# Kernel optimization log

Measured on AMD Instinct MI355X. Metric: run time of the kernel, lower is better.

## Reference

```python
import jax, jax.numpy as jnp
import numpy as np

E = 8          # n_experts
TOP_K = 2      # n_active_experts


def setup_inputs() -> dict:
    key = jax.random.key(0)
    ks = jax.random.split(key, 9)
    B, S, D, H = 4, 2048, 2048, 1408
    w = 0.02  # weight scale for numerical stability
    return {
        "x": jax.random.normal(ks[0], (B, S, D), dtype=jnp.float32),
        "gate_w": jax.random.normal(ks[1], (E, D), dtype=jnp.float32) * w,
        "expert_bias": jnp.zeros((E,), dtype=jnp.float32),
        "Wg": jax.random.normal(ks[2], (E, H, D), dtype=jnp.float32) * w,
        "Wu": jax.random.normal(ks[3], (E, H, D), dtype=jnp.float32) * w,
        "Wd": jax.random.normal(ks[4], (E, D, H), dtype=jnp.float32) * w,
        "Ws_g": jax.random.normal(ks[5], (H, D), dtype=jnp.float32) * w,
        "Ws_u": jax.random.normal(ks[6], (H, D), dtype=jnp.float32) * w,
        "Ws_d": jax.random.normal(ks[7], (D, H), dtype=jnp.float32) * w,
    }


def _swiglu(x, wg, wu, wd):
    # torch Linear layout: y = x @ W.T
    return (jax.nn.silu(x @ wg.T) * (x @ wu.T)) @ wd.T


def reference(x, gate_w, expert_bias, Wg, Wu, Wd, Ws_g, Ws_u, Ws_d):
    B, S, D = x.shape
    flat = x.reshape(-1, D)                      # [N, D]
    N = flat.shape[0]

    logits = flat @ gate_w.T                     # [N, E]
    probs = jax.nn.softmax(logits, axis=-1)
    biased = logits + expert_bias
    _, top_idx = jax.lax.top_k(biased, TOP_K)    # [N, K] (bias used only for selection)
    top_w = jnp.take_along_axis(probs, top_idx, axis=-1)
    top_w = top_w / jnp.sum(top_w, axis=-1, keepdims=True)

    # dense per-token combine weights: cw[n, e] = sum_k top_w[n,k] * (top_idx[n,k]==e)
    rows = jnp.arange(N)[:, None]
    cw = jnp.zeros((N, E), dtype=flat.dtype).at[rows, top_idx].add(top_w)

    out = jnp.zeros_like(flat)
    for e in range(E):  # fixed small expert count; equivalent to gather/scatter dispatch
        out = out + cw[:, e:e + 1] * _swiglu(flat, Wg[e], Wu[e], Wd[e])

    out = out + _swiglu(flat, Ws_g, Ws_u, Ws_d)  # shared expert
    return out.reshape(B, S, D)
```

## Files before the change

### kernel.cpp

```cpp
#include <hip/hip_runtime.h>
#include <hip/hip_bf16.h>

#define N_TOK 8192
#define DDIM  2048
#define HDIM  1408
#define ROWS_R 16384
#define ROWS_T 24576
#define MAXTILES 104
#define BM 256
#define BK 64

typedef unsigned short u16;
typedef unsigned int   u32;
typedef __bf16 bf16x8 __attribute__((ext_vector_type(8)));
typedef float  f32x4  __attribute__((ext_vector_type(4)));

__device__ __forceinline__ u16 f2bf(float f) {
  union { float f; u32 u; } v; v.f = f;
  u32 u = v.u;
  return (u16)((u + 0x7fffu + ((u >> 16) & 1u)) >> 16);
}
__device__ __forceinline__ float bf2f(u16 b) {
  union { u32 u; float f; } v; v.u = ((u32)b) << 16; return v.f;
}

typedef __attribute__((address_space(1))) void gvoid;
typedef __attribute__((address_space(3))) void lvoid;
__device__ __forceinline__ void gload16(const void* g, void* l) {
  __builtin_amdgcn_global_load_lds((gvoid*)g, (lvoid*)l, 16, 0, 0);
}

#define BAR __builtin_amdgcn_s_barrier()
#define SP1 __builtin_amdgcn_s_setprio(1)
#define SP0 __builtin_amdgcn_s_setprio(0)
#define LGK0 do { asm volatile("s_waitcnt lgkmcnt(0)" ::: "memory"); \
                  __builtin_amdgcn_sched_barrier(0); } while (0)
#define VMCNT(n) asm volatile("s_waitcnt vmcnt(" #n ")" ::: "memory")

#define READ_A8(base, mb) { \
  _Pragma("unroll") for (int m_ = 0; m_ < 4; ++m_) { \
    int r_ = wr * 128 + ((mb) + m_) * 16 + l15; \
    _Pragma("unroll") for (int kk_ = 0; kk_ < 2; ++kk_) { \
      int cch_ = kk_ * 4 + lhi; \
      af[m_ * 2 + kk_] = *(const bf16x8*)((const char*)(base) + r_ * 128 + ((cch_ ^ (r_ & 7)) * 16)); } } }

#define READ_B4(base, nb) { \
  _Pragma("unroll") for (int n_ = 0; n_ < 2; ++n_) { \
    int r_ = wc * 64 + ((nb) + n_) * 16 + l15; \
    _Pragma("unroll") for (int kk_ = 0; kk_ < 2; ++kk_) { \
      int cch_ = kk_ * 4 + lhi; \
      bf[((nb) + n_) * 2 + kk_] = *(const bf16x8*)((const char*)(base) + r_ * 128 + ((cch_ ^ (r_ & 7)) * 16)); } } }

#define MM16(mb, nb) { \
  _Pragma("unroll") for (int m_ = 0; m_ < 4; ++m_) \
  _Pragma("unroll") for (int n_ = 0; n_ < 2; ++n_) \
  _Pragma("unroll") for (int kk_ = 0; kk_ < 2; ++kk_) \
    acc[(mb) + m_][(nb) + n_] = __builtin_amdgcn_mfma_f32_16x16x32_bf16( \
        af[m_ * 2 + kk_], bf[((nb) + n_) * 2 + kk_], acc[(mb) + m_][(nb) + n_], 0, 0, 0); }

__global__ void k_gate(const float* __restrict__ x, const float* __restrict__ gw,
                       const float* __restrict__ bias, int* __restrict__ tok_idx,
                       float* __restrict__ wts, int* __restrict__ counts,
                       u16* __restrict__ xb) {
  int lane = threadIdx.x & 63;
  int n = blockIdx.x * 4 + (threadIdx.x >> 6);
  const float* xr = x + (size_t)n * DDIM;
  u16* xbr = xb + (size_t)n * DDIM;
  float acc[8];
#pragma unroll
  for (int e = 0; e < 8; ++e) acc[e] = 0.f;
#pragma unroll 2
  for (int j0 = 0; j0 < DDIM; j0 += 256) {
    float4 xv = *(const float4*)(xr + j0 + lane * 4);
    u32 p0 = (u32)f2bf(xv.x) | ((u32)f2bf(xv.y) << 16);
    u32 p1 = (u32)f2bf(xv.z) | ((u32)f2bf(xv.w) << 16);
    *(uint2*)(xbr + j0 + lane * 4) = make_uint2(p0, p1);
#pragma unroll
    for (int e = 0; e < 8; ++e) {
      float4 gv = *(const float4*)(gw + e * DDIM + j0 + lane * 4);
      acc[e] += xv.x * gv.x + xv.y * gv.y + xv.z * gv.z + xv.w * gv.w;
    }
  }
#pragma unroll
  for (int e = 0; e < 8; ++e) {
#pragma unroll
    for (int off = 32; off > 0; off >>= 1) acc[e] += __shfl_xor(acc[e], off);
  }
  if (lane == 0) {
    float m = acc[0];
    for (int e = 1; e < 8; ++e) m = fmaxf(m, acc[e]);
    float p[8];
    for (int e = 0; e < 8; ++e) p[e] = expf(acc[e] - m);
    float b0[8];
    for (int e = 0; e < 8; ++e) b0[e] = acc[e] + bias[e];
    int i0 = 0;
    for (int e = 1; e < 8; ++e) if (b0[e] > b0[i0]) i0 = e;
    int i1 = (i0 == 0) ? 1 : 0;
    for (int e = 0; e < 8; ++e) if (e != i0 && b0[e] > b0[i1]) i1 = e;
    float w0 = p[i0], w1 = p[i1], inv = 1.f / (w0 + w1);
    tok_idx[2 * n] = i0; tok_idx[2 * n + 1] = i1;
    wts[2 * n] = w0 * inv; wts[2 * n + 1] = w1 * inv;
    atomicAdd(&counts[i0], 1); atomicAdd(&counts[i1], 1);
  }
}

__global__ void k_scan(const int* __restrict__ counts, int* __restrict__ offsets,
                       int* __restrict__ cursors, int* __restrict__ ntiles,
                       int4* __restrict__ tiles) {
  if (threadIdx.x != 0 || blockIdx.x != 0) return;
  int off = 0, idx = 0;
  for (int e = 0; e < 8; ++e) {
    offsets[e] = off; cursors[e] = 0;
    int T = counts[e];
    for (int r = 0; r < T; r += BM) {
      int nr = T - r; if (nr > BM) nr = BM;
      tiles[idx++] = make_int4(e, off + r, nr, 0);
    }
    off += T;
  }
  offsets[8] = off;
  for (int r = 0; r < N_TOK; r += BM)
    tiles[idx++] = make_int4(8, ROWS_R + r, BM, 0);
  *ntiles = idx;
}

__global__ void k_build(const int* __restrict__ tok_idx, const int* __restrict__ offsets,
                        int* __restrict__ cursors, int* __restrict__ token_ids,
                        int* __restrict__ pos) {
  int n = blockIdx.x * blockDim.x + threadIdx.x;
  if (n >= N_TOK) return;
#pragma unroll
  for (int s = 0; s < 2; ++s) {
    int e = tok_idx[2 * n + s];
    int p = offsets[e] + atomicAdd(&cursors[e], 1);
    token_ids[p] = n;
    pos[2 * n + s] = p;
  }
  token_ids[ROWS_R + n] = n;
}

__global__ void k_convall(const float* __restrict__ Wg, const float* __restrict__ Wsg,
                          const float* __restrict__ Wu, const float* __restrict__ Wsu,
                          const float* __restrict__ Wd, const float* __restrict__ Wsd,
                          u16* __restrict__ wgb, u16* __restrict__ wub, u16* __restrict__ wdb) {
  const long PER = (long)9 * HDIM * DDIM / 8;
  const long BIG = (long)8 * HDIM * DDIM / 8;
  const long TOT = 3 * PER;
  long stride = (long)gridDim.x * blockDim.x;
  for (long i = (long)blockIdx.x * blockDim.x + threadIdx.x; i < TOT; i += stride) {
    int g = (int)(i / PER);
    long r = i - (long)g * PER;
    const float* src; u16* dst;
    if (g == 0)      { dst = wgb; src = (r < BIG) ? Wg + r * 8 : Wsg + (r - BIG) * 8; }
    else if (g == 1) { dst = wub; src = (r < BIG) ? Wu + r * 8 : Wsu + (r - BIG) * 8; }
    else             { dst = wdb; src = (r < BIG) ? Wd + r * 8 : Wsd + (r - BIG) * 8; }
    float4 a = ((const float4*)src)[0], b = ((const float4*)src)[1];
    u32 p0 = (u32)f2bf(a.x) | ((u32)f2bf(a.y) << 16);
    u32 p1 = (u32)f2bf(a.z) | ((u32)f2bf(a.w) << 16);
    u32 p2 = (u32)f2bf(b.x) | ((u32)f2bf(b.y) << 16);
    u32 p3 = (u32)f2bf(b.z) | ((u32)f2bf(b.w) << 16);
    ((uint4*)dst)[r] = make_uint4(p0, p1, p2, p3);
  }
}

__global__ __launch_bounds__(512, 2) void k_gemm1(
    const u16* __restrict__ xb, const u16* __restrict__ wgb, const u16* __restrict__ wub,
    const int* __restrict__ token_ids, const int* __restrict__ ntiles,
    const int4* __restrict__ tiles, u16* __restrict__ h) {
  __shared__ u16 As[2][BM * BK];
  __shared__ u16 Bs[2][BM * BK];

  int ntl = *ntiles;
  int nwg = (HDIM / 128) * ntl;
  int bid = blockIdx.x;
  if (bid >= nwg) return;
  int q8 = nwg >> 3, r8 = nwg & 7;
  int xcd = bid & 7, pp = bid >> 3;
  int lid = (xcd < r8 ? xcd * (q8 + 1) : r8 * (q8 + 1) + (xcd - r8) * q8) + pp;
  int bx = lid / ntl, tile = lid - bx * ntl;

  int4 tl = tiles[tile];
  int set = tl.x, grow = tl.y, nrows = tl.z;

  int t = threadIdx.x;
  int wid = t >> 6, lane = t & 63;
  int wr = wid >> 2, wc = wid & 3;
  int l15 = lane & 15, lhi = lane >> 4;

  const u16* aptr[4];
#pragma unroll
  for (int i = 0; i < 4; ++i) {
    int chunk = i * 512 + t;
    int r = chunk >> 3, cc = chunk & 7;
    int c = cc ^ (r & 7);
    int rr = r < nrows ? r : nrows - 1;
    int tok = token_ids[grow + rr];
    aptr[i] = xb + (size_t)tok * DDIM + c * 8;
  }
  const u16* bptr[4];
#pragma unroll
  for (int i = 0; i < 4; ++i) {
    int chunk = i * 512 + t;
    int r = chunk >> 3, cc = chunk & 7;
    int c = cc ^ (r & 7);
    int group = r >> 4;
    int wrow = bx * 128 + (group >> 1) * 16 + (r & 15);
    const u16* base = (group & 1) ? wub : wgb;
    bptr[i] = base + (size_t)set * (HDIM * DDIM) + (size_t)wrow * DDIM + c * 8;
  }

#define ISSUE_A0(b, k0) { gload16(aptr[0] + (k0), (char*)As[b] + (size_t)t * 16); \
                          gload16(aptr[1] + (k0), (char*)As[b] + (size_t)(512 + t) * 16); }
#define ISSUE_A1(b, k0) { gload16(aptr[2] + (k0), (char*)As[b] + (size_t)(1024 + t) * 16); \
                          gload16(aptr[3] + (k0), (char*)As[b] + (size_t)(1536 + t) * 16); }
#define ISSUE_B0(b, k0) { gload16(bptr[0] + (k0), (char*)Bs[b] + (size_t)t * 16); \
                          gload16(bptr[1] + (k0), (char*)Bs[b] + (size_t)(512 + t) * 16); }
#define ISSUE_B1(b, k0) { gload16(bptr[2] + (k0), (char*)Bs[b] + (size_t)(1024 + t) * 16); \
                          gload16(bptr[3] + (k0), (char*)Bs[b] + (size_t)(1536 + t) * 16); }

  f32x4 acc[8][4];
  f32x4 z = {0.f, 0.f, 0.f, 0.f};
#pragma unroll
  for (int m = 0; m < 8; ++m)
#pragma unroll
    for (int n = 0; n < 4; ++n) acc[m][n] = z;

  bf16x8 af[8], bf[8];
  const int NK = DDIM / BK;

  VMCNT(0);
  ISSUE_A0(0, 0); ISSUE_A1(0, 0); ISSUE_B0(0, 0); ISSUE_B1(0, 0);
  VMCNT(0); BAR;

  for (int kt = 0; kt < NK - 1; ++kt) {
    int cur = kt & 1, nxt = cur ^ 1;
    int k1 = (kt + 1) * BK;
    READ_A8(As[cur], 0); READ_B4(Bs[cur], 0);
    ISSUE_A0(nxt, k1); ISSUE_B0(nxt, k1);
    BAR; LGK0;
    SP1; MM16(0, 0); SP0; BAR;
    READ_B4(Bs[cur], 2);
    ISSUE_A1(nxt, k1); ISSUE_B1(nxt, k1);
    BAR; LGK0;
    SP1; MM16(0, 2); SP0; BAR;
    READ_A8(As[cur], 4);
    BAR; LGK0;
    SP1; MM16(4, 0); MM16(4, 2); SP0;
    VMCNT(0); BAR;
  }
  {
    int cur = (NK - 1) & 1;
    READ_A8(As[cur], 0); READ_B4(Bs[cur], 0); READ_B4(Bs[cur], 2);
    LGK0;
    SP1; MM16(0, 0); MM16(0, 2); SP0;
    READ_A8(As[cur], 4);
    LGK0;
    SP1; MM16(4, 0); MM16(4, 2); SP0;
  }

#pragma unroll
  for (int m = 0; m < 8; ++m) {
#pragma unroll
    for (int j = 0; j < 2; ++j) {
      int col = bx * 128 + (wc * 2 + j) * 16 + l15;
#pragma unroll
      for (int qq = 0; qq < 4; ++qq) {
        int rl = wr * 128 + m * 16 + lhi * 4 + qq;
        if (rl < nrows) {
          float g = acc[m][2 * j][qq], u = acc[m][2 * j + 1][qq];
          float hv = g / (1.f + expf(-g)) * u;
          h[(size_t)(grow + rl) * HDIM + col] = f2bf(hv);
        }
      }
    }
  }
#undef ISSUE_A0
#undef ISSUE_A1
#undef ISSUE_B0
#undef ISSUE_B1
}

__global__ __launch_bounds__(512, 2) void k_gemm2(
    const u16* __restrict__ h, const u16* __restrict__ wdb,
    const int* __restrict__ ntiles, const int4* __restrict__ tiles,
    u16* __restrict__ y) {
  __shared__ u16 As[2][BM * BK];
  __shared__ u16 Bs[2][BM * BK];

  int ntl = *ntiles;
  int nwg = (DDIM / 256) * ntl;
  int bid = blockIdx.x;
  if (bid >= nwg) return;
  int q8 = nwg >> 3, r8 = nwg & 7;
  int xcd = bid & 7, pp = bid >> 3;
  int lid = (xcd < r8 ? xcd * (q8 + 1) : r8 * (q8 + 1) + (xcd - r8) * q8) + pp;
  int bx = lid / ntl, tile = lid - bx * ntl;

  int4 tl = tiles[tile];
  int set = tl.x, grow = tl.y, nrows = tl.z;

  int t = threadIdx.x;
  int wid = t >> 6, lane = t & 63;
  int wr = wid >> 2, wc = wid & 3;
  int l15 = lane & 15, lhi = lane >> 4;

  const u16* aptr[4];
  const u16* bptr[4];
#pragma unroll
  for (int i = 0; i < 4; ++i) {
    int chunk = i * 512 + t;
    int r = chunk >> 3, cc = chunk & 7;
    int c = cc ^ (r & 7);
    aptr[i] = h + (size_t)(grow + r) * HDIM + c * 8;
    bptr[i] = wdb + (size_t)set * (DDIM * HDIM) + (size_t)(bx * 256 + r) * HDIM + c * 8;
  }

#define ISSUE_A0(b, k0) { gload16(aptr[0] + (k0), (char*)As[b] + (size_t)t * 16); \
                          gload16(aptr[1] + (k0), (char*)As[b] + (size_t)(512 + t) * 16); }
#define ISSUE_A1(b, k0) { gload16(aptr[2] + (k0), (char*)As[b] + (size_t)(1024 + t) * 16); \
                          gload16(aptr[3] + (k0), (char*)As[b] + (size_t)(1536 + t) * 16); }
#define ISSUE_B0(b, k0) { gload16(bptr[0] + (k0), (char*)Bs[b] + (size_t)t * 16); \
                          gload16(bptr[1] + (k0), (char*)Bs[b] + (size_t)(512 + t) * 16); }
#define ISSUE_B1(b, k0) { gload16(bptr[2] + (k0), (char*)Bs[b] + (size_t)(1024 + t) * 16); \
                          gload16(bptr[3] + (k0), (char*)Bs[b] + (size_t)(1536 + t) * 16); }

  f32x4 acc[8][4];
  f32x4 z = {0.f, 0.f, 0.f, 0.f};
#pragma unroll
  for (int m = 0; m < 8; ++m)
#pragma unroll
    for (int n = 0; n < 4; ++n) acc[m][n] = z;

  bf16x8 af[8], bf[8];
  const int NK2 = HDIM / BK;

  VMCNT(0);
  ISSUE_A0(0, 0); ISSUE_A1(0, 0); ISSUE_B0(0, 0); ISSUE_B1(0, 0);
  VMCNT(0); BAR;

  for (int kt = 0; kt < NK2 - 1; ++kt) {
    int cur = kt & 1, nxt = cur ^ 1;
    int k1 = (kt + 1) * BK;
    READ_A8(As[cur], 0); READ_B4(Bs[cur], 0);
    ISSUE_A0(nxt, k1); ISSUE_B0(nxt, k1);
    BAR; LGK0;
    SP1; MM16(0, 0); SP0; BAR;
    READ_B4(Bs[cur], 2);
    ISSUE_A1(nxt, k1); ISSUE_B1(nxt, k1);
    BAR; LGK0;
    SP1; MM16(0, 2); SP0; BAR;
    READ_A8(As[cur], 4);
    BAR; LGK0;
    SP1; MM16(4, 0); MM16(4, 2); SP0;
    VMCNT(0); BAR;
  }
  {
    int cur = (NK2 - 1) & 1;
    READ_A8(As[cur], 0); READ_B4(Bs[cur], 0); READ_B4(Bs[cur], 2);
    LGK0;
    SP1; MM16(0, 0); MM16(0, 2); SP0;
    READ_A8(As[cur], 4);
    LGK0;
    SP1; MM16(4, 0); MM16(4, 2); SP0;
  }

#pragma unroll
  for (int m = 0; m < 8; ++m) {
#pragma unroll
    for (int n = 0; n < 4; ++n) {
      int col = bx * 256 + wc * 64 + n * 16 + l15;
#pragma unroll
      for (int qq = 0; qq < 4; ++qq) {
        int rl = wr * 128 + m * 16 + lhi * 4 + qq;
        if (rl < nrows)
          y[(size_t)(grow + rl) * DDIM + col] = f2bf(acc[m][n][qq]);
      }
    }
  }
#undef ISSUE_A0
#undef ISSUE_A1
#undef ISSUE_B0
#undef ISSUE_B1
}

__global__ void k_comb(const u16* __restrict__ y, const int* __restrict__ pos,
                       const float* __restrict__ wts, float* __restrict__ out) {
  int n = blockIdx.x;
  int c8 = threadIdx.x;
  int p0 = pos[2 * n], p1 = pos[2 * n + 1];
  float w0 = wts[2 * n], w1 = wts[2 * n + 1];
  uint4 a = ((const uint4*)(y + (size_t)p0 * DDIM))[c8];
  uint4 b = ((const uint4*)(y + (size_t)p1 * DDIM))[c8];
  uint4 c = ((const uint4*)(y + (size_t)(ROWS_R + n) * DDIM))[c8];
  float* o = out + (size_t)n * DDIM + c8 * 8;
#pragma unroll
  for (int j = 0; j < 4; ++j) {
    u32 ua = ((const u32*)&a)[j], ub = ((const u32*)&b)[j], uc = ((const u32*)&c)[j];
    o[2 * j]     = w0 * bf2f((u16)(ua & 0xffff)) + w1 * bf2f((u16)(ub & 0xffff)) + bf2f((u16)(uc & 0xffff));
    o[2 * j + 1] = w0 * bf2f((u16)(ua >> 16))    + w1 * bf2f((u16)(ub >> 16))    + bf2f((u16)(uc >> 16));
  }
}

extern "C" void kernel_launch(void* const* d_in, const int* in_sizes, int n_in,
                              void* d_out, int out_size, void* d_ws, size_t ws_size,
                              hipStream_t stream) {
  const float* x    = (const float*)d_in[0];
  const float* gw   = (const float*)d_in[1];
  const float* bias = (const float*)d_in[2];
  const float* Wg   = (const float*)d_in[3];
  const float* Wu   = (const float*)d_in[4];
  const float* Wd   = (const float*)d_in[5];
  const float* Wsg  = (const float*)d_in[6];
  const float* Wsu  = (const float*)d_in[7];
  const float* Wsd  = (const float*)d_in[8];
  float* out = (float*)d_out;

  char* ws = (char*)d_ws;
  size_t off = 0;
  auto alloc = [&](size_t bytes) -> void* {
    void* p = ws + off;
    off += (bytes + 255) & ~(size_t)255;
    return p;
  };
  u16* xb  = (u16*)alloc((size_t)N_TOK * DDIM * 2);
  u16* wgb = (u16*)alloc((size_t)9 * HDIM * DDIM * 2);
  u16* wub = (u16*)alloc((size_t)9 * HDIM * DDIM * 2);
  u16* wdb = (u16*)alloc((size_t)9 * DDIM * HDIM * 2);
  u16* h   = (u16*)alloc((size_t)ROWS_T * HDIM * 2);
  u16* y   = (u16*)alloc((size_t)ROWS_T * DDIM * 2);
  int*   token_ids = (int*)alloc(ROWS_T * 4);
  int*   tok_idx   = (int*)alloc(N_TOK * 2 * 4);
  int*   pos       = (int*)alloc(N_TOK * 2 * 4);
  float* wts       = (float*)alloc(N_TOK * 2 * 4);
  int*   counts  = (int*)alloc(8 * 4);
  int*   offsets = (int*)alloc(9 * 4);
  int*   cursors = (int*)alloc(8 * 4);
  int*   ntiles  = (int*)alloc(4);
  int4*  tiles   = (int4*)alloc(MAXTILES * 16);

  hipMemsetAsync(counts, 0, 8 * 4, stream);
  k_gate<<<N_TOK / 4, 256, 0, stream>>>(x, gw, bias, tok_idx, wts, counts, xb);
  k_scan<<<1, 64, 0, stream>>>(counts, offsets, cursors, ntiles, tiles);
  k_build<<<(N_TOK + 255) / 256, 256, 0, stream>>>(tok_idx, offsets, cursors, token_ids, pos);

  k_convall<<<4096, 256, 0, stream>>>(Wg, Wsg, Wu, Wsu, Wd, Wsd, wgb, wub, wdb);

  k_gemm1<<<(HDIM / 128) * MAXTILES, 512, 0, stream>>>(xb, wgb, wub, token_ids, ntiles, tiles, h);
  k_gemm2<<<(DDIM / 256) * MAXTILES, 512, 0, stream>>>(h, wdb, ntiles, tiles, y);
  k_comb<<<N_TOK, 256, 0, stream>>>(y, pos, wts, out);
}
```

Measured before the change: 948.0 us.

## Software-pipeline LDS fragment reads across K tiles with double-buffered registers in both GEMMs

Replaces the per-K-tile schedule (read fragments, wait lgkmcnt(0), compute) with a register double-buffered pipeline. A fragments alternate between two register sets by quarter, and B fragments plus the first A quarter of the next tile are prefetched from LDS while the current tile's last MFMAs run. The global-to-LDS loads for the whole next tile are issued in one STAGE call, and barriers drop from five to two per tile. Explicit lgkmcnt waits are gone, so LDS-read ordering is left to the compiler. This adds register pressure under the 512-thread, 2-blocks-per-CU bounds and risks correctness if the odd/even tile unrolling is wrong.

```diff
diff --git a/kernel.cpp b/kernel.cpp
--- a/kernel.cpp
+++ b/kernel.cpp
@@ -30,33 +30,41 @@
   __builtin_amdgcn_global_load_lds((gvoid*)g, (lvoid*)l, 16, 0, 0);
 }
 
-#define BAR __builtin_amdgcn_s_barrier()
+#define BARF asm volatile("s_barrier" ::: "memory")
 #define SP1 __builtin_amdgcn_s_setprio(1)
 #define SP0 __builtin_amdgcn_s_setprio(0)
-#define LGK0 do { asm volatile("s_waitcnt lgkmcnt(0)" ::: "memory"); \
-                  __builtin_amdgcn_sched_barrier(0); } while (0)
+#define SB0 __builtin_amdgcn_sched_barrier(0)
 #define VMCNT(n) asm volatile("s_waitcnt vmcnt(" #n ")" ::: "memory")
 
-#define READ_A8(base, mb) { \
-  _Pragma("unroll") for (int m_ = 0; m_ < 4; ++m_) { \
-    int r_ = wr * 128 + ((mb) + m_) * 16 + l15; \
+#define RDA4(cc, q, dst) { \
+  _Pragma("unroll") for (int m_ = 0; m_ < 2; ++m_) { \
+    int r_ = wr * 128 + ((q) * 2 + m_) * 16 + l15; \
     _Pragma("unroll") for (int kk_ = 0; kk_ < 2; ++kk_) { \
       int cch_ = kk_ * 4 + lhi; \
-      af[m_ * 2 + kk_] = *(const bf16x8*)((const char*)(base) + r_ * 128 + ((cch_ ^ (r_ & 7)) * 16)); } } }
-
-#define READ_B4(base, nb) { \
-  _Pragma("unroll") for (int n_ = 0; n_ < 2; ++n_) { \
-    int r_ = wc * 64 + ((nb) + n_) * 16 + l15; \
+      (dst)[m_ * 2 + kk_] = *(const bf16x8*)((const char*)As[cc] + r_ * 128 + ((cch_ ^ (r_ & 7)) * 16)); } } }
+
+#define RDB8(cc, dst) { \
+  _Pragma("unroll") for (int n_ = 0; n_ < 4; ++n_) { \
+    int r_ = wc * 64 + n_ * 16 + l15; \
     _Pragma("unroll") for (int kk_ = 0; kk_ < 2; ++kk_) { \
       int cch_ = kk_ * 4 + lhi; \
-      bf[((nb) + n_) * 2 + kk_] = *(const bf16x8*)((const char*)(base) + r_ * 128 + ((cch_ ^ (r_ & 7)) * 16)); } } }
-
-#define MM16(mb, nb) { \
-  _Pragma("unroll") for (int m_ = 0; m_ < 4; ++m_) \
-  _Pragma("unroll") for (int n_ = 0; n_ < 2; ++n_) \
+      (dst)[n_ * 2 + kk_] = *(const bf16x8*)((const char*)Bs[cc] + r_ * 128 + ((cch_ ^ (r_ & 7)) * 16)); } } }
+
+#define MMQ(q, AF, BB) { \
+  _Pragma("unroll") for (int m_ = 0; m_ < 2; ++m_) \
+  _Pragma("unroll") for (int n_ = 0; n_ < 4; ++n_) \
   _Pragma("unroll") for (int kk_ = 0; kk_ < 2; ++kk_) \
-    acc[(mb) + m_][(nb) + n_] = __builtin_amdgcn_mfma_f32_16x16x32_bf16( \
-        af[m_ * 2 + kk_], bf[((nb) + n_) * 2 + kk_], acc[(mb) + m_][(nb) + n_], 0, 0, 0); }
+    acc[(q) * 2 + m_][n_] = __builtin_amdgcn_mfma_f32_16x16x32_bf16( \
+        (AF)[m_ * 2 + kk_], (BB)[n_ * 2 + kk_], acc[(q) * 2 + m_][n_], 0, 0, 0); }
+
+#define TILEB(cc, k0next, BC, BN) { \
+  BARF; \
+  STAGE(cc ^ 1, k0next); \
+  RDA4(cc, 1, afB); SB0; SP1; MMQ(0, afA, BC); SP0; \
+  RDA4(cc, 2, afA); SB0; SP1; MMQ(1, afB, BC); SP0; \
+  VMCNT(0); BARF; \
+  RDA4(cc, 3, afB); SB0; SP1; MMQ(2, afA, BC); SP0; \
+  RDB8(cc ^ 1, BN); RDA4(cc ^ 1, 0, afA); SB0; SP1; MMQ(3, afB, BC); SP0; }
 
 __global__ void k_gate(const float* __restrict__ x, const float* __restrict__ gw,
                        const float* __restrict__ bias, int* __restrict__ tok_idx,
@@ -209,14 +217,15 @@
     bptr[i] = base + (size_t)set * (HDIM * DDIM) + (size_t)wrow * DDIM + c * 8;
   }
 
-#define ISSUE_A0(b, k0) { gload16(aptr[0] + (k0), (char*)As[b] + (size_t)t * 16); \
-                          gload16(aptr[1] + (k0), (char*)As[b] + (size_t)(512 + t) * 16); }
-#define ISSUE_A1(b, k0) { gload16(aptr[2] + (k0), (char*)As[b] + (size_t)(1024 + t) * 16); \
-                          gload16(aptr[3] + (k0), (char*)As[b] + (size_t)(1536 + t) * 16); }
-#define ISSUE_B0(b, k0) { gload16(bptr[0] + (k0), (char*)Bs[b] + (size_t)t * 16); \
-                          gload16(bptr[1] + (k0), (char*)Bs[b] + (size_t)(512 + t) * 16); }
-#define ISSUE_B1(b, k0) { gload16(bptr[2] + (k0), (char*)Bs[b] + (size_t)(1024 + t) * 16); \
-                          gload16(bptr[3] + (k0), (char*)Bs[b] + (size_t)(1536 + t) * 16); }
+#define STAGE(cc, k0) { \
+  gload16(aptr[0] + (k0), (char*)As[cc] + (size_t)t * 16); \
+  gload16(aptr[1] + (k0), (char*)As[cc] + (size_t)(512 + t) * 16); \
+  gload16(aptr[2] + (k0), (char*)As[cc] + (size_t)(1024 + t) * 16); \
+  gload16(aptr[3] + (k0), (char*)As[cc] + (size_t)(1536 + t) * 16); \
+  gload16(bptr[0] + (k0), (char*)Bs[cc] + (size_t)t * 16); \
+  gload16(bptr[1] + (k0), (char*)Bs[cc] + (size_t)(512 + t) * 16); \
+  gload16(bptr[2] + (k0), (char*)Bs[cc] + (size_t)(1024 + t) * 16); \
+  gload16(bptr[3] + (k0), (char*)Bs[cc] + (size_t)(1536 + t) * 16); }
 
   f32x4 acc[8][4];
   f32x4 z = {0.f, 0.f, 0.f, 0.f};
@@ -225,38 +234,24 @@
 #pragma unroll
     for (int n = 0; n < 4; ++n) acc[m][n] = z;
 
-  bf16x8 af[8], bf[8];
+  bf16x8 afA[4], afB[4], b0[8], b1[8];
   const int NK = DDIM / BK;
 
   VMCNT(0);
-  ISSUE_A0(0, 0); ISSUE_A1(0, 0); ISSUE_B0(0, 0); ISSUE_B1(0, 0);
-  VMCNT(0); BAR;
-
-  for (int kt = 0; kt < NK - 1; ++kt) {
-    int cur = kt & 1, nxt = cur ^ 1;
-    int k1 = (kt + 1) * BK;
-    READ_A8(As[cur], 0); READ_B4(Bs[cur], 0);
-    ISSUE_A0(nxt, k1); ISSUE_B0(nxt, k1);
-    BAR; LGK0;
-    SP1; MM16(0, 0); SP0; BAR;
-    READ_B4(Bs[cur], 2);
-    ISSUE_A1(nxt, k1); ISSUE_B1(nxt, k1);
-    BAR; LGK0;
-    SP1; MM16(0, 2); SP0; BAR;
-    READ_A8(As[cur], 4);
-    BAR; LGK0;
-    SP1; MM16(4, 0); MM16(4, 2); SP0;
-    VMCNT(0); BAR;
-  }
-  {
-    int cur = (NK - 1) & 1;
-    READ_A8(As[cur], 0); READ_B4(Bs[cur], 0); READ_B4(Bs[cur], 2);
-    LGK0;
-    SP1; MM16(0, 0); MM16(0, 2); SP0;
-    READ_A8(As[cur], 4);
-    LGK0;
-    SP1; MM16(4, 0); MM16(4, 2); SP0;
-  }
+  STAGE(0, 0);
+  VMCNT(0); BARF;
+  RDB8(0, b0); RDA4(0, 0, afA);
+
+  for (int kt = 0; kt < NK - 2; kt += 2) {
+    TILEB(0, (kt + 1) * BK, b0, b1);
+    TILEB(1, (kt + 2) * BK, b1, b0);
+  }
+  TILEB(0, (NK - 1) * BK, b0, b1);
+  BARF;
+  RDA4(1, 1, afB); SB0; SP1; MMQ(0, afA, b1); SP0;
+  RDA4(1, 2, afA); SB0; SP1; MMQ(1, afB, b1); SP0;
+  RDA4(1, 3, afB); SB0; SP1; MMQ(2, afA, b1); SP0;
+  SP1; MMQ(3, afB, b1); SP0;
 
 #pragma unroll
   for (int m = 0; m < 8; ++m) {
@@ -274,10 +269,7 @@
       }
     }
   }
-#undef ISSUE_A0
-#undef ISSUE_A1
-#undef ISSUE_B0
-#undef ISSUE_B1
+#undef STAGE
 }
 
 __global__ __launch_bounds__(512, 2) void k_gemm2(
@@ -315,14 +307,15 @@
     bptr[i] = wdb + (size_t)set * (DDIM * HDIM) + (size_t)(bx * 256 + r) * HDIM + c * 8;
   }
 
-#define ISSUE_A0(b, k0) { gload16(aptr[0] + (k0), (char*)As[b] + (size_t)t * 16); \
-                          gload16(aptr[1] + (k0), (char*)As[b] + (size_t)(512 + t) * 16); }
-#define ISSUE_A1(b, k0) { gload16(aptr[2] + (k0), (char*)As[b] + (size_t)(1024 + t) * 16); \
-                          gload16(aptr[3] + (k0), (char*)As[b] + (size_t)(1536 + t) * 16); }
-#define ISSUE_B0(b, k0) { gload16(bptr[0] + (k0), (char*)Bs[b] + (size_t)t * 16); \
-                          gload16(bptr[1] + (k0), (char*)Bs[b] + (size_t)(512 + t) * 16); }
-#define ISSUE_B1(b, k0) { gload16(bptr[2] + (k0), (char*)Bs[b] + (size_t)(1024 + t) * 16); \
-                          gload16(bptr[3] + (k0), (char*)Bs[b] + (size_t)(1536 + t) * 16); }
+#define STAGE(cc, k0) { \
+  gload16(aptr[0] + (k0), (char*)As[cc] + (size_t)t * 16); \
+  gload16(aptr[1] + (k0), (char*)As[cc] + (size_t)(512 + t) * 16); \
+  gload16(aptr[2] + (k0), (char*)As[cc] + (size_t)(1024 + t) * 16); \
+  gload16(aptr[3] + (k0), (char*)As[cc] + (size_t)(1536 + t) * 16); \
+  gload16(bptr[0] + (k0), (char*)Bs[cc] + (size_t)t * 16); \
+  gload16(bptr[1] + (k0), (char*)Bs[cc] + (size_t)(512 + t) * 16); \
+  gload16(bptr[2] + (k0), (char*)Bs[cc] + (size_t)(1024 + t) * 16); \
+  gload16(bptr[3] + (k0), (char*)Bs[cc] + (size_t)(1536 + t) * 16); }
 
   f32x4 acc[8][4];
   f32x4 z = {0.f, 0.f, 0.f, 0.f};
@@ -331,38 +324,24 @@
 #pragma unroll
     for (int n = 0; n < 4; ++n) acc[m][n] = z;
 
-  bf16x8 af[8], bf[8];
-  const int NK2 = HDIM / BK;
+  bf16x8 afA[4], afB[4], b0[8], b1[8];
+  const int NK = HDIM / BK;
 
   VMCNT(0);
-  ISSUE_A0(0, 0); ISSUE_A1(0, 0); ISSUE_B0(0, 0); ISSUE_B1(0, 0);
-  VMCNT(0); BAR;
-
-  for (int kt = 0; kt < NK2 - 1; ++kt) {
-    int cur = kt & 1, nxt = cur ^ 1;
-    int k1 = (kt + 1) * BK;
-    READ_A8(As[cur], 0); READ_B4(Bs[cur], 0);
-    ISSUE_A0(nxt, k1); ISSUE_B0(nxt, k1);
-    BAR; LGK0;
-    SP1; MM16(0, 0); SP0; BAR;
-    READ_B4(Bs[cur], 2);
-    ISSUE_A1(nxt, k1); ISSUE_B1(nxt, k1);
-    BAR; LGK0;
-    SP1; MM16(0, 2); SP0; BAR;
-    READ_A8(As[cur], 4);
-    BAR; LGK0;
-    SP1; MM16(4, 0); MM16(4, 2); SP0;
-    VMCNT(0); BAR;
-  }
-  {
-    int cur = (NK2 - 1) & 1;
-    READ_A8(As[cur], 0); READ_B4(Bs[cur], 0); READ_B4(Bs[cur], 2);
-    LGK0;
-    SP1; MM16(0, 0); MM16(0, 2); SP0;
-    READ_A8(As[cur], 4);
-    LGK0;
-    SP1; MM16(4, 0); MM16(4, 2); SP0;
-  }
+  STAGE(0, 0);
+  VMCNT(0); BARF;
+  RDB8(0, b0); RDA4(0, 0, afA);
+
+  for (int kt = 0; kt < NK - 2; kt += 2) {
+    TILEB(0, (kt + 1) * BK, b0, b1);
+    TILEB(1, (kt + 2) * BK, b1, b0);
+  }
+  TILEB(0, (NK - 1) * BK, b0, b1);
+  BARF;
+  RDA4(1, 1, afB); SB0; SP1; MMQ(0, afA, b1); SP0;
+  RDA4(1, 2, afA); SB0; SP1; MMQ(1, afB, b1); SP0;
+  RDA4(1, 3, afB); SB0; SP1; MMQ(2, afA, b1); SP0;
+  SP1; MMQ(3, afB, b1); SP0;
 
 #pragma unroll
   for (int m = 0; m < 8; ++m) {
@@ -377,10 +356,7 @@
       }
     }
   }
-#undef ISSUE_A0
-#undef ISSUE_A1
-#undef ISSUE_B0
-#undef ISSUE_B1
+#undef STAGE
 }
 
 __global__ void k_comb(const u16* __restrict__ y, const int* __restrict__ pos,
```

After: 1.123 ms. 18.4% more time.
